# Optimization experiments

Hardware: AMD Instinct MI355X
Metric: run time of the kernel (lower is better)

## Reference

```python
import jax, jax.numpy as jnp
import numpy as np

# Module hyperparameters (from init_kwargs)
A, B, K, P, STRIDE, PAD, ITERS = 32, 32, 3, 4, 2, 0, 3
C = P * P          # 16, input pose matrix size
D = P * P          # 16, output pose matrix size
KK = K * K         # 9
KKA = KK * A       # 288
EPS = 1e-8


def setup_inputs() -> dict:
    key = jax.random.key(0)
    k1, k2 = jax.random.split(key)
    pose = jax.random.normal(k1, (4, A * C, 32, 32), dtype=jnp.float32)
    # kaiming-uniform-like scale for W [kkA, B*D, C]
    W = jax.random.normal(k2, (KKA, B * D, C), dtype=jnp.float32) / np.sqrt(C).astype(np.float32)
    return {"pose": pose, "W": W}


def _unfold(x):
    # Equivalent of F.unfold(x, K, stride=STRIDE, padding=0), channel-major,
    # kernel positions (ki, kj) fastest -> (b, ch, KK, l)
    b, ch, h, w = x.shape
    oh = (h - K) // STRIDE + 1
    ow = (w - K) // STRIDE + 1
    hi = STRIDE * (oh - 1) + 1
    wi = STRIDE * (ow - 1) + 1
    cols = [x[:, :, i:i + hi:STRIDE, j:j + wi:STRIDE]
            for i in range(K) for j in range(K)]
    p = jnp.stack(cols, axis=2)  # (b, ch, KK, oh, ow)
    return p.reshape(b, ch, KK, oh * ow), oh, ow


def _squash(s):
    # standard capsule squash along last (pose) dim
    n2 = jnp.sum(s * s, axis=-1, keepdims=True)
    return s * n2 / ((1.0 + n2) * jnp.sqrt(n2 + EPS))


def reference(pose, W):
    b = pose.shape[0]
    p, oh, ow = _unfold(pose)               # (b, A*C, KK, l)
    l = oh * ow
    # view(b,A,C,kk,l) -> permute(0,4,3,1,2) -> (b,l,kk,A,C) -> (b,l,kkA,C)
    p = p.reshape(b, A, C, KK, l).transpose(0, 4, 3, 1, 2).reshape(b, l, KKA, C)
    # votes: W [kkA, B*D, C] @ pose [..., C, 1]
    votes = jnp.einsum('kdc,blkc->blkd', W, p).reshape(b, l, KKA, B, D)
    # routing-by-agreement
    logits = jnp.zeros((b, l, KKA, B, 1), dtype=pose.dtype)
    v = None
    for _ in range(ITERS):
        c = jax.nn.softmax(logits, axis=3)              # over B output capsules
        s = jnp.sum(c * votes, axis=2, keepdims=True)   # (b, l, 1, B, D)
        v = _squash(s)
        logits = logits + jnp.sum(v * votes, axis=-1, keepdims=True)
    v = v[:, :, 0].reshape(b, l, B * D)     # (b, l, B*D)
    v = v.transpose(0, 2, 1)                # (b, B*D, l)
    return v.reshape(b, B * D, oh, ow)
```

## Files before the change

### kernel.cpp

```cpp
#include <hip/hip_runtime.h>
#include <math.h>

#define KC   18
#define KPC  16
#define NP   928
#define NPT  29

typedef __attribute__((ext_vector_type(8)))  short short8;
typedef __attribute__((ext_vector_type(16))) float f32x16;

__device__ __forceinline__ unsigned short f2bf(float x) {
    union { float f; unsigned u; } v; v.f = x;
    unsigned r = v.u + 0x7fffu + ((v.u >> 16) & 1u);
    return (unsigned short)(r >> 16);
}
__device__ __forceinline__ float bf2f(unsigned short h) {
    union { unsigned u; float f; } v; v.u = ((unsigned)h) << 16;
    return v.f;
}

__global__ void wprep(const float* __restrict__ W,
                      unsigned short* __restrict__ Whi,
                      unsigned short* __restrict__ Wlo)
{
    int idx = (blockIdx.x * 256 + threadIdx.x) * 4;
    float4 x = *(const float4*)(W + idx);
    ushort4 h, l;
    h.x = f2bf(x.x); l.x = f2bf(x.x - bf2f(h.x));
    h.y = f2bf(x.y); l.y = f2bf(x.y - bf2f(h.y));
    h.z = f2bf(x.z); l.z = f2bf(x.z - bf2f(h.z));
    h.w = f2bf(x.w); l.w = f2bf(x.w - bf2f(h.w));
    *(ushort4*)(Whi + idx) = h;
    *(ushort4*)(Wlo + idx) = l;
}

__global__ void unfold(const float* __restrict__ pose,
                       unsigned short* __restrict__ Phi,
                       unsigned short* __restrict__ Plo)
{
    int bid = blockIdx.x;
    int k = bid / 58;
    int chunk = bid % 58;
    int t = threadIdx.x;
    int c = t & 15;
    int pos = chunk * 16 + (t >> 4);
    int a = k & 31;
    int kk = k >> 5;
    int ki = kk / 3, kj = kk % 3;
    float val = 0.f;
    if (pos < 900) {
        int batch = pos / 225;
        int rr = pos - batch * 225;
        int oi = rr / 15, oj = rr - (rr / 15) * 15;
        val = pose[(((size_t)batch * 512 + a * 16 + c) * 32 + (oi * 2 + ki)) * 32 + (oj * 2 + kj)];
    }
    unsigned short h = f2bf(val);
    unsigned short l = f2bf(val - bf2f(h));
    size_t o = ((size_t)k * NP + pos) * 16 + c;
    Phi[o] = h;
    Plo[o] = l;
}

template<int ITER>
__global__ __launch_bounds__(512) void route(const unsigned short* __restrict__ Whi,
                                             const unsigned short* __restrict__ Wlo,
                                             const unsigned short* __restrict__ Phi,
                                             const unsigned short* __restrict__ Plo,
                                             const float* __restrict__ V,
                                             unsigned short* __restrict__ part)
{
    __shared__ float2 smb[2][8][32];

    const int bid = blockIdx.x;
    const int kc = bid % KC;
    const int pt = bid / KC;
    const int t = threadIdx.x;
    const int w = t >> 6;
    const int l = t & 63;
    const int col = l & 31;
    const int h = l >> 5;
    const int gpos = pt * 32 + col;
    const int bd0 = w * 64;

    float vf[2][16];
    if constexpr (ITER > 0) {
        const float* vp = V + (size_t)gpos * 512 + bd0 + 4 * h;
#pragma unroll
        for (int m = 0; m < 2; ++m)
#pragma unroll
            for (int q = 0; q < 4; ++q) {
                float4 x = *(const float4*)(vp + m * 32 + 8 * q);
                vf[m][q * 4 + 0] = x.x; vf[m][q * 4 + 1] = x.y;
                vf[m][q * 4 + 2] = x.z; vf[m][q * 4 + 3] = x.w;
            }
    }

    f32x16 s[2];
#pragma unroll
    for (int m = 0; m < 2; ++m)
#pragma unroll
        for (int r = 0; r < 16; ++r) s[m][r] = 0.f;

    for (int kl = 0; kl < KPC; ++kl) {
        const int k = kc * KPC + kl;
        size_t ab = ((size_t)k * 512 + bd0 + col) * 16 + 8 * h;
        short8 ah0 = *(const short8*)(Whi + ab);
        short8 ah1 = *(const short8*)(Whi + ab + 512);
        short8 al0 = *(const short8*)(Wlo + ab);
        short8 al1 = *(const short8*)(Wlo + ab + 512);
        size_t bb = ((size_t)k * NP + gpos) * 16 + 8 * h;
        short8 bh = *(const short8*)(Phi + bb);
        short8 bl = *(const short8*)(Plo + bb);

        if constexpr (ITER == 0) {
            s[0] = __builtin_amdgcn_mfma_f32_32x32x16_bf16(ah0, bh, s[0], 0, 0, 0);
            s[0] = __builtin_amdgcn_mfma_f32_32x32x16_bf16(ah0, bl, s[0], 0, 0, 0);
            s[0] = __builtin_amdgcn_mfma_f32_32x32x16_bf16(al0, bh, s[0], 0, 0, 0);
            s[1] = __builtin_amdgcn_mfma_f32_32x32x16_bf16(ah1, bh, s[1], 0, 0, 0);
            s[1] = __builtin_amdgcn_mfma_f32_32x32x16_bf16(ah1, bl, s[1], 0, 0, 0);
            s[1] = __builtin_amdgcn_mfma_f32_32x32x16_bf16(al1, bh, s[1], 0, 0, 0);
        } else {
            f32x16 v[2];
#pragma unroll
            for (int m = 0; m < 2; ++m)
#pragma unroll
                for (int r = 0; r < 16; ++r) v[m][r] = 0.f;
            v[0] = __builtin_amdgcn_mfma_f32_32x32x16_bf16(ah0, bh, v[0], 0, 0, 0);
            v[0] = __builtin_amdgcn_mfma_f32_32x32x16_bf16(ah0, bl, v[0], 0, 0, 0);
            v[0] = __builtin_amdgcn_mfma_f32_32x32x16_bf16(al0, bh, v[0], 0, 0, 0);
            v[1] = __builtin_amdgcn_mfma_f32_32x32x16_bf16(ah1, bh, v[1], 0, 0, 0);
            v[1] = __builtin_amdgcn_mfma_f32_32x32x16_bf16(ah1, bl, v[1], 0, 0, 0);
            v[1] = __builtin_amdgcn_mfma_f32_32x32x16_bf16(al1, bh, v[1], 0, 0, 0);

            float lp[4] = {0.f, 0.f, 0.f, 0.f};
#pragma unroll
            for (int m = 0; m < 2; ++m)
#pragma unroll
                for (int q = 0; q < 4; ++q)
#pragma unroll
                    for (int i = 0; i < 4; ++i)
                        lp[m * 2 + (q >> 1)] = fmaf(v[m][q * 4 + i], vf[m][q * 4 + i],
                                                    lp[m * 2 + (q >> 1)]);
#pragma unroll
            for (int j = 0; j < 4; ++j) lp[j] += __shfl_xor(lp[j], 32);

            float mw = fmaxf(fmaxf(lp[0], lp[1]), fmaxf(lp[2], lp[3]));
            float ex[4], sw = 0.f;
#pragma unroll
            for (int j = 0; j < 4; ++j) { ex[j] = __expf(lp[j] - mw); sw += ex[j]; }
            if (h == 0) smb[kl & 1][w][col] = make_float2(mw, sw);
            __syncthreads();
            float2 z[8];
            float M = -1e30f;
#pragma unroll
            for (int ww = 0; ww < 8; ++ww) { z[ww] = smb[kl & 1][ww][col]; M = fmaxf(M, z[ww].x); }
            float denom = 0.f;
#pragma unroll
            for (int ww = 0; ww < 8; ++ww) denom += z[ww].y * __expf(z[ww].x - M);
            float scale = __expf(mw - M) / denom;
            float cw[4];
#pragma unroll
            for (int j = 0; j < 4; ++j) cw[j] = ex[j] * scale;

#pragma unroll
            for (int m = 0; m < 2; ++m)
#pragma unroll
                for (int q = 0; q < 4; ++q)
#pragma unroll
                    for (int i = 0; i < 4; ++i)
                        s[m][q * 4 + i] = fmaf(cw[m * 2 + (q >> 1)], v[m][q * 4 + i],
                                               s[m][q * 4 + i]);
        }
    }

    const float mult = (ITER == 0) ? (1.0f / 32.0f) : 1.0f;
#pragma unroll
    for (int m = 0; m < 2; ++m)
#pragma unroll
        for (int q = 0; q < 4; ++q)
#pragma unroll
            for (int i = 0; i < 4; ++i) {
                int bd = bd0 + m * 32 + 8 * q + 4 * h + i;
                part[((size_t)(kc * 512 + bd)) * NP + gpos] = f2bf(s[m][q * 4 + i] * mult);
            }
}

template<int ITER>
__global__ __launch_bounds__(256) void squash(const unsigned short* __restrict__ part,
                                              float* __restrict__ V,
                                              float* __restrict__ out)
{
    int bid = blockIdx.x;
    int pt = bid >> 2, bg = bid & 3;
    int t = threadIdx.x;
    int pos = pt * 32 + (t & 31);
    int b = bg * 8 + (t >> 5);

    float s[16];
#pragma unroll
    for (int d = 0; d < 16; ++d) s[d] = 0.f;
    for (int kc = 0; kc < KC; ++kc) {
        const unsigned short* pp = part + ((size_t)(kc * 512 + b * 16)) * NP + pos;
#pragma unroll
        for (int d = 0; d < 16; ++d) s[d] += bf2f(pp[(size_t)d * NP]);
    }
    float n2 = 0.f;
#pragma unroll
    for (int d = 0; d < 16; ++d) n2 = fmaf(s[d], s[d], n2);
    float scale = n2 / ((1.0f + n2) * sqrtf(n2 + 1e-8f));

    if constexpr (ITER < 2) {
        float* vp = V + (size_t)pos * 512 + b * 16;
#pragma unroll
        for (int d = 0; d < 16; ++d) {
            float val = s[d] * scale;
            if constexpr (ITER == 0) vp[d] = val;
            else                     vp[d] += val;
        }
    } else {
        if (pos < 900) {
            int batch = pos / 225;
            int opos = pos - batch * 225;
            float* op = out + ((size_t)(batch * 512 + b * 16)) * 225 + opos;
#pragma unroll
            for (int d = 0; d < 16; ++d) op[(size_t)d * 225] = s[d] * scale;
        }
    }
}

extern "C" void kernel_launch(void* const* d_in, const int* in_sizes, int n_in,
                              void* d_out, int out_size, void* d_ws, size_t ws_size,
                              hipStream_t stream)
{
    const float* pose = (const float*)d_in[0];
    const float* Wg   = (const float*)d_in[1];
    float* out = (float*)d_out;
    char* ws = (char*)d_ws;
    unsigned short* Whi  = (unsigned short*)(ws);
    unsigned short* Wlo  = (unsigned short*)(ws + 4718592);
    unsigned short* Phi  = (unsigned short*)(ws + 9437184);
    unsigned short* Plo  = (unsigned short*)(ws + 17989632);
    unsigned short* part = (unsigned short*)(ws + 26542080);
    float* V             = (float*)(ws + 43646976);

    wprep<<<2304, 256, 0, stream>>>(Wg, Whi, Wlo);
    unfold<<<288 * 58, 256, 0, stream>>>(pose, Phi, Plo);

    route<0><<<NPT * KC, 512, 0, stream>>>(Whi, Wlo, Phi, Plo, V, part);
    squash<0><<<116, 256, 0, stream>>>(part, V, out);
    route<1><<<NPT * KC, 512, 0, stream>>>(Whi, Wlo, Phi, Plo, V, part);
    squash<1><<<116, 256, 0, stream>>>(part, V, out);
    route<2><<<NPT * KC, 512, 0, stream>>>(Whi, Wlo, Phi, Plo, V, part);
    squash<2><<<116, 256, 0, stream>>>(part, V, out);
}
```

Before: 266.3 us.

## Prefetch next-k operands in route, stage unfold through LDS, reorder blocks

The route kernel now loads the W and P fragments for the next k step before running the MFMAs for the current one, interleaves the two accumulator chains, and replaces __syncthreads with a raw waitcnt plus barrier. Block order is changed so consecutive blocks share a k-chunk (the same W), and launch bounds ask for two blocks per CU. The unfold kernel is restructured to stage a 32x32 tile per (batch, a) in LDS and emit all nine kernel positions from it, using 128 large blocks instead of many small gather blocks. The prefetch reads one step past the end of the chunk on the last iteration (an unused load that can fall outside the buffers for the last chunk). The unfold rewrite cuts redundant global reads but leaves only 128 blocks of parallelism.

```diff
diff --git a/kernel.cpp b/kernel.cpp
--- a/kernel.cpp
+++ b/kernel.cpp
@@ -34,46 +34,62 @@
     *(ushort4*)(Wlo + idx) = l;
 }
 
-__global__ void unfold(const float* __restrict__ pose,
-                       unsigned short* __restrict__ Phi,
-                       unsigned short* __restrict__ Plo)
-{
-    int bid = blockIdx.x;
-    int k = bid / 58;
-    int chunk = bid % 58;
-    int t = threadIdx.x;
-    int c = t & 15;
-    int pos = chunk * 16 + (t >> 4);
-    int a = k & 31;
-    int kk = k >> 5;
-    int ki = kk / 3, kj = kk % 3;
-    float val = 0.f;
-    if (pos < 900) {
-        int batch = pos / 225;
-        int rr = pos - batch * 225;
-        int oi = rr / 15, oj = rr - (rr / 15) * 15;
-        val = pose[(((size_t)batch * 512 + a * 16 + c) * 32 + (oi * 2 + ki)) * 32 + (oj * 2 + kj)];
-    }
-    unsigned short h = f2bf(val);
-    unsigned short l = f2bf(val - bf2f(h));
-    size_t o = ((size_t)k * NP + pos) * 16 + c;
-    Phi[o] = h;
-    Plo[o] = l;
+__global__ __launch_bounds__(256) void unfold(const float* __restrict__ pose,
+                                              unsigned short* __restrict__ Phi,
+                                              unsigned short* __restrict__ Plo)
+{
+    __shared__ float lds[16 * 1057];
+    const int bid = blockIdx.x;
+    const int batch = bid >> 5;
+    const int a = bid & 31;
+    const int t = threadIdx.x;
+
+    const float* src = pose + ((size_t)batch * 512 + a * 16) * 1024;
+#pragma unroll
+    for (int c = 0; c < 16; ++c) {
+        float4 v = *(const float4*)(src + c * 1024 + t * 4);
+        float* d = &lds[c * 1057 + (t >> 3) * 33 + (t & 7) * 4];
+        d[0] = v.x; d[1] = v.y; d[2] = v.z; d[3] = v.w;
+    }
+    __syncthreads();
+
+    const int c = t & 15;
+    const int px = t >> 4;
+    for (int it = 0; it < 15; ++it) {
+        int pos = it * 16 + px;
+        bool ok = pos < 225;
+        int pc = ok ? pos : 224;
+        int oi = pc / 15, oj = pc - oi * 15;
+#pragma unroll
+        for (int ki = 0; ki < 3; ++ki)
+#pragma unroll
+            for (int kj = 0; kj < 3; ++kj) {
+                float val = lds[c * 1057 + (oi * 2 + ki) * 33 + (oj * 2 + kj)];
+                unsigned short hh = f2bf(val);
+                unsigned short ll = f2bf(val - bf2f(hh));
+                if (ok) {
+                    size_t o = ((size_t)((ki * 3 + kj) * 32 + a) * NP
+                                + batch * 225 + pos) * 16 + c;
+                    Phi[o] = hh;
+                    Plo[o] = ll;
+                }
+            }
+    }
 }
 
 template<int ITER>
-__global__ __launch_bounds__(512) void route(const unsigned short* __restrict__ Whi,
-                                             const unsigned short* __restrict__ Wlo,
-                                             const unsigned short* __restrict__ Phi,
-                                             const unsigned short* __restrict__ Plo,
-                                             const float* __restrict__ V,
-                                             unsigned short* __restrict__ part)
+__global__ __launch_bounds__(512, 2) void route(const unsigned short* __restrict__ Whi,
+                                                const unsigned short* __restrict__ Wlo,
+                                                const unsigned short* __restrict__ Phi,
+                                                const unsigned short* __restrict__ Plo,
+                                                const float* __restrict__ V,
+                                                unsigned short* __restrict__ part)
 {
     __shared__ float2 smb[2][8][32];
 
     const int bid = blockIdx.x;
-    const int kc = bid % KC;
-    const int pt = bid / KC;
+    const int pt = bid % NPT;
+    const int kc = bid / NPT;
     const int t = threadIdx.x;
     const int w = t >> 6;
     const int l = t & 63;
@@ -101,23 +117,35 @@
 #pragma unroll
         for (int r = 0; r < 16; ++r) s[m][r] = 0.f;
 
+    const size_t k0 = (size_t)kc * KPC;
+    const unsigned short* pWh = Whi + (k0 * 512 + bd0 + col) * 16 + 8 * h;
+    const unsigned short* pWl = Wlo + (k0 * 512 + bd0 + col) * 16 + 8 * h;
+    const unsigned short* pPh = Phi + (k0 * NP + gpos) * 16 + 8 * h;
+    const unsigned short* pPl = Plo + (k0 * NP + gpos) * 16 + 8 * h;
+
+    short8 ah0 = *(const short8*)(pWh);
+    short8 ah1 = *(const short8*)(pWh + 512);
+    short8 al0 = *(const short8*)(pWl);
+    short8 al1 = *(const short8*)(pWl + 512);
+    short8 bh  = *(const short8*)(pPh);
+    short8 bl  = *(const short8*)(pPl);
+
     for (int kl = 0; kl < KPC; ++kl) {
-        const int k = kc * KPC + kl;
-        size_t ab = ((size_t)k * 512 + bd0 + col) * 16 + 8 * h;
-        short8 ah0 = *(const short8*)(Whi + ab);
-        short8 ah1 = *(const short8*)(Whi + ab + 512);
-        short8 al0 = *(const short8*)(Wlo + ab);
-        short8 al1 = *(const short8*)(Wlo + ab + 512);
-        size_t bb = ((size_t)k * NP + gpos) * 16 + 8 * h;
-        short8 bh = *(const short8*)(Phi + bb);
-        short8 bl = *(const short8*)(Plo + bb);
+        const int nw = (kl + 1) * 8192;
+        const int np = (kl + 1) * 14848;
+        short8 nah0 = *(const short8*)(pWh + nw);
+        short8 nah1 = *(const short8*)(pWh + nw + 512);
+        short8 nal0 = *(const short8*)(pWl + nw);
+        short8 nal1 = *(const short8*)(pWl + nw + 512);
+        short8 nbh  = *(const short8*)(pPh + np);
+        short8 nbl  = *(const short8*)(pPl + np);
 
         if constexpr (ITER == 0) {
             s[0] = __builtin_amdgcn_mfma_f32_32x32x16_bf16(ah0, bh, s[0], 0, 0, 0);
+            s[1] = __builtin_amdgcn_mfma_f32_32x32x16_bf16(ah1, bh, s[1], 0, 0, 0);
             s[0] = __builtin_amdgcn_mfma_f32_32x32x16_bf16(ah0, bl, s[0], 0, 0, 0);
+            s[1] = __builtin_amdgcn_mfma_f32_32x32x16_bf16(ah1, bl, s[1], 0, 0, 0);
             s[0] = __builtin_amdgcn_mfma_f32_32x32x16_bf16(al0, bh, s[0], 0, 0, 0);
-            s[1] = __builtin_amdgcn_mfma_f32_32x32x16_bf16(ah1, bh, s[1], 0, 0, 0);
-            s[1] = __builtin_amdgcn_mfma_f32_32x32x16_bf16(ah1, bl, s[1], 0, 0, 0);
             s[1] = __builtin_amdgcn_mfma_f32_32x32x16_bf16(al1, bh, s[1], 0, 0, 0);
         } else {
             f32x16 v[2];
@@ -126,10 +154,10 @@
 #pragma unroll
                 for (int r = 0; r < 16; ++r) v[m][r] = 0.f;
             v[0] = __builtin_amdgcn_mfma_f32_32x32x16_bf16(ah0, bh, v[0], 0, 0, 0);
+            v[1] = __builtin_amdgcn_mfma_f32_32x32x16_bf16(ah1, bh, v[1], 0, 0, 0);
             v[0] = __builtin_amdgcn_mfma_f32_32x32x16_bf16(ah0, bl, v[0], 0, 0, 0);
+            v[1] = __builtin_amdgcn_mfma_f32_32x32x16_bf16(ah1, bl, v[1], 0, 0, 0);
             v[0] = __builtin_amdgcn_mfma_f32_32x32x16_bf16(al0, bh, v[0], 0, 0, 0);
-            v[1] = __builtin_amdgcn_mfma_f32_32x32x16_bf16(ah1, bh, v[1], 0, 0, 0);
-            v[1] = __builtin_amdgcn_mfma_f32_32x32x16_bf16(ah1, bl, v[1], 0, 0, 0);
             v[1] = __builtin_amdgcn_mfma_f32_32x32x16_bf16(al1, bh, v[1], 0, 0, 0);
 
             float lp[4] = {0.f, 0.f, 0.f, 0.f};
@@ -149,7 +177,7 @@
 #pragma unroll
             for (int j = 0; j < 4; ++j) { ex[j] = __expf(lp[j] - mw); sw += ex[j]; }
             if (h == 0) smb[kl & 1][w][col] = make_float2(mw, sw);
-            __syncthreads();
+            asm volatile("s_waitcnt lgkmcnt(0)\n\ts_barrier" ::: "memory");
             float2 z[8];
             float M = -1e30f;
 #pragma unroll
@@ -171,6 +199,8 @@
                         s[m][q * 4 + i] = fmaf(cw[m * 2 + (q >> 1)], v[m][q * 4 + i],
                                                s[m][q * 4 + i]);
         }
+
+        ah0 = nah0; ah1 = nah1; al0 = nal0; al1 = nal1; bh = nbh; bl = nbl;
     }
 
     const float mult = (ITER == 0) ? (1.0f / 32.0f) : 1.0f;
@@ -244,7 +274,7 @@
     float* V             = (float*)(ws + 43646976);
 
     wprep<<<2304, 256, 0, stream>>>(Wg, Whi, Wlo);
-    unfold<<<288 * 58, 256, 0, stream>>>(pose, Phi, Plo);
+    unfold<<<128, 256, 0, stream>>>(pose, Phi, Plo);
 
     route<0><<<NPT * KC, 512, 0, stream>>>(Whi, Wlo, Phi, Plo, V, part);
     squash<0><<<116, 256, 0, stream>>>(part, V, out);
```

Measured after the change: 245.0 us. 8.0% less time.
